# Optimization experiments

Hardware: AMD Instinct MI355X
Metric: run time of the kernel (lower is better)

The kernel has to match this reference:

```python
import jax, jax.numpy as jnp
from jax import lax
import numpy as np

B, S = 64, 16
GD, LD, PD, HD, CD = 64, 32, 8, 64, 64  # global, local, periodic, hidden, coder dims
TWO_PI = 6.283185307179586


def _conv(x, w, b):
    y = lax.conv_general_dilated(x, w, (2, 2), [(1, 1), (1, 1)])
    return y + b[None, :, None, None]


def _deconv(x, w, b):
    # torch ConvTranspose2d(k=4, s=2, p=1); w is [in, out, 4, 4].
    # Equivalent: dilate lhs by 2, pad k-1-p=2 each side, conv with flipped kernel.
    wt = jnp.flip(w, (2, 3)).transpose(1, 0, 2, 3)  # -> OIHW
    y = lax.conv_general_dilated(x, wt, (1, 1), [(2, 2), (2, 2)], lhs_dilation=(2, 2))
    return y + b[None, :, None, None]


def _bn(x, g, b, eps=1e-5):
    # training-mode BatchNorm2d (biased variance, per-channel affine)
    m = x.mean((0, 2, 3), keepdims=True)
    v = x.var((0, 2, 3), keepdims=True)
    return (x - m) * lax.rsqrt(v + eps) * g[None, :, None, None] + b[None, :, None, None]


def setup_inputs() -> dict:
    key = jax.random.key(0)
    ks = iter(jax.random.split(key, 40))
    n = lambda shape, s=0.02: jax.random.normal(next(ks), shape, jnp.float32) * s
    return {
        "Z_l": jax.random.normal(next(ks), (B, LD, S, S), jnp.float32),
        "Z_g": jax.random.normal(next(ks), (B, GD, S, S), jnp.float32),
        "imgs": jax.random.normal(next(ks), (B, 3, 128, 128), jnp.float32),
        "phi": jax.random.uniform(next(ks), (B, PD, 1, 1), jnp.float32),
        "lW": n((HD, GD)), "lb": n((HD,)),
        "l1W": n((PD, HD)), "l1b": n((PD,)),
        "l2W": n((PD, HD)), "l2b": n((PD,)),
        "cod_w0": n((64, 3, 4, 4)), "cod_b0": n((64,)),
        "cod_g0": 1.0 + n((64,)), "cod_be0": n((64,)),
        "cod_w1": n((128, 64, 4, 4)), "cod_b1": n((128,)),
        "cod_g1": 1.0 + n((128,)), "cod_be1": n((128,)),
        "cod_w2": n((CD, 128, 4, 4)), "cod_b2": n((CD,)),
        "gen_w0": n((CD + LD + GD + PD, 256, 4, 4)), "gen_b0": n((256,)),
        "gen_g0": 1.0 + n((256,)), "gen_be0": n((256,)),
        "gen_w1": n((256, 128, 4, 4)), "gen_b1": n((128,)),
        "gen_g1": 1.0 + n((128,)), "gen_be1": n((128,)),
        "gen_w2": n((128, 3, 4, 4)), "gen_b2": n((3,)),
    }


def reference(Z_l, Z_g, imgs, phi, lW, lb, l1W, l1b, l2W, l2b,
              cod_w0, cod_b0, cod_g0, cod_be0, cod_w1, cod_b1, cod_g1, cod_be1,
              cod_w2, cod_b2,
              gen_w0, gen_b0, gen_g0, gen_be0, gen_w1, gen_b1, gen_g1, gen_be1,
              gen_w2, gen_b2):
    # --- image coder: [B,3,128,128] -> [B,CD,16,16] ---
    h = jax.nn.leaky_relu(_bn(_conv(imgs, cod_w0, cod_b0), cod_g0, cod_be0), 0.2)
    h = jax.nn.leaky_relu(_bn(_conv(h, cod_w1, cod_b1), cod_g1, cod_be1), 0.2)
    Z_c = jnp.tanh(_conv(h, cod_w2, cod_b2))
    # --- periodic noise: vectorized outer-product replacing S*S python loop ---
    zg = Z_g[:, :, 0, 0]                       # [B, GD]
    x = jax.nn.relu(zg @ lW.T + lb)            # [B, HD]
    K1 = x @ l1W.T + l1b                       # [B, PD]
    K2 = x @ l2W.T + l2b                       # [B, PD]
    idx = jnp.arange(S, dtype=jnp.float32)
    wave = K1[:, :, None, None] * idx[:, None] + K2[:, :, None, None] * idx[None, :]
    Z_p = jnp.sin(wave + phi * TWO_PI)         # [B, PD, S, S]
    # --- generator ---
    Z = jnp.concatenate((Z_c, Z_l, Z_g, Z_p), axis=1)  # [B, 168, 16, 16]
    h = jax.nn.relu(_bn(_deconv(Z, gen_w0, gen_b0), gen_g0, gen_be0))
    h = jax.nn.relu(_bn(_deconv(h, gen_w1, gen_b1), gen_g1, gen_be1))
    return jnp.tanh(_deconv(h, gen_w2, gen_b2))        # [B, 3, 128, 128]
```

## Files before the change

### kernel.cpp

```cpp
#include <hip/hip_runtime.h>
#include <hip/hip_bf16.h>

#define TWO_PI_F 6.2831853071795864769f

typedef __attribute__((ext_vector_type(8))) __bf16 bf16x8;
typedef __attribute__((ext_vector_type(4))) float f32x4;

#define NREP 32

__device__ __forceinline__ float bf2f_raw(unsigned short u) {
    return __uint_as_float(((unsigned int)u) << 16);
}
__device__ __forceinline__ unsigned short f2bf(float f) {
    unsigned int u = __float_as_uint(f);
    unsigned int r = (u + 0x7FFFu + ((u >> 16) & 1u)) >> 16;
    return (unsigned short)r;
}
__device__ __forceinline__ float loadIn(const void* p, size_t i, bool f32) {
    return f32 ? ((const float*)p)[i] : bf2f_raw(((const unsigned short*)p)[i]);
}

__device__ __forceinline__ uint4 bn_fuse8(uint4 v, const float* __restrict__ sc,
                                          const float* __restrict__ sh, int c0, float slope) {
    unsigned short us[8];
    *(uint4*)us = v;
#pragma unroll
    for (int k = 0; k < 8; ++k) {
        float f = bf2f_raw(us[k]) * sc[c0 + k] + sh[c0 + k];
        f = f > 0.f ? f : slope * f;
        us[k] = f2bf(f);
    }
    return *(const uint4*)us;
}

__device__ __forceinline__ float kq_reduce(float v) {
    v += __shfl_xor(v, 16, 64);
    v += __shfl_xor(v, 32, 64);
    return v;
}

static constexpr size_t OFF_WC0 = 0;
static constexpr size_t OFF_WG2 = 3072;
static constexpr size_t OFF_P   = 9216;
static constexpr size_t OFF_CB0 = OFF_P + 0;
static constexpr size_t OFF_CG0 = OFF_P + 64;
static constexpr size_t OFF_CBE0= OFF_P + 128;
static constexpr size_t OFF_CB1 = OFF_P + 192;
static constexpr size_t OFF_CG1 = OFF_P + 320;
static constexpr size_t OFF_CBE1= OFF_P + 448;
static constexpr size_t OFF_CB2 = OFF_P + 576;
static constexpr size_t OFF_GB0 = OFF_P + 640;
static constexpr size_t OFF_GG0 = OFF_P + 896;
static constexpr size_t OFF_GBE0= OFF_P + 1152;
static constexpr size_t OFF_GB1 = OFF_P + 1408;
static constexpr size_t OFF_GG1 = OFF_P + 1536;
static constexpr size_t OFF_GBE1= OFF_P + 1664;
static constexpr size_t OFF_GB2 = OFF_P + 1792;
static constexpr size_t OFF_SSUM  = OFF_P + 2048;
static constexpr size_t OFF_SSQ   = OFF_SSUM + NREP * 576;
static constexpr size_t OFF_SCALE = OFF_SSQ + NREP * 576;
static constexpr size_t OFF_SHIFT = OFF_SCALE + 576;
static constexpr size_t OFF_K12   = OFF_SHIFT + 576;
static constexpr size_t OFF_FLAG  = OFF_K12 + 1024;
static constexpr size_t FP32_END  = OFF_FLAG + 16;
static constexpr size_t UXT = 2 * FP32_END;
static constexpr size_t UYT = UXT + 16777216;
static constexpr size_t UZT = UYT + 8388608;
static constexpr size_t UW0 = UYT + 33554432;
static constexpr size_t UW1 = UW0 + 786432;
static constexpr size_t UWC1 = UW1 + 524288;
static constexpr size_t UWC2 = UWC1 + 131072;
static constexpr size_t UW2 = UWC2 + 131072;
static constexpr size_t WS_END_USHORT = UW2 + 32768;
static constexpr size_t WS_NEED_BYTES = WS_END_USHORT * 2;


__global__ void detect_kernel(const unsigned short* __restrict__ imgs, int* __restrict__ flag) {
    int t = threadIdx.x;
    unsigned short u = imgs[t];
    int e = (u >> 7) & 0xFF;
    unsigned long long b = __ballot(e >= 0xC0);
    __shared__ int cnt[4];
    if ((t & 63) == 0) cnt[t >> 6] = __popcll(b);
    __syncthreads();
    if (t == 0) flag[0] = (cnt[0] + cnt[1] + cnt[2] + cnt[3] >= 4) ? 1 : 0;
}

struct CvtJobs {
    const void* src[16];
    float* dst[16];
    int off[17];
};

__global__ void cvt_all_kernel(CvtJobs J, int total, const int* __restrict__ flg) {
    int i = blockIdx.x * 256 + threadIdx.x;
    if (i >= total) return;
    bool f32 = flg[0] != 0;
    int k = 0;
#pragma unroll
    for (int t = 0; t < 15; ++t) { if (i >= J.off[t + 1]) k = t + 1; }
    int r = i - J.off[k];
    J.dst[k][r] = loadIn(J.src[k], r, f32);
}

__global__ void zero_kernel(float* p, int n) {
    int i = blockIdx.x * 256 + threadIdx.x;
    if (i < n) p[i] = 0.f;
}

__global__ void pack_w2_kernel(const void* __restrict__ src, unsigned short* __restrict__ dst,
                               int ICreal, int ICP, int OC, const int* __restrict__ flg) {
    bool f32 = flg[0] != 0;
    int i = blockIdx.x * 256 + threadIdx.x;
    int total = 16 * OC * ICP;
    if (i >= total) return;
    int jj = i & 7;
    int lane = (i >> 3) & 63;
    int j = (i >> 9) & 3;
    int t3 = i >> 11;
    int NK = ICP / 32;
    int kc = t3 % NK;
    int t4 = t3 / NK;
    int NOCT = OC / 64;
    int oct = t4 % NOCT;
    int ktap = t4 / NOCT;
    int kq = lane >> 4, n = lane & 15;
    int ic = kc * 32 + kq * 8 + jj;
    int oc = oct * 64 + n * 4 + j;
    unsigned short v = 0;
    if (ic < ICreal) v = f2bf(loadIn(src, ((size_t)(ic * OC + oc) << 4) + ktap, f32));
    dst[i] = v;
}

__global__ void pack_w2s_kernel(const void* __restrict__ src, unsigned short* __restrict__ dst,
                                int ICP, int OCreal, const int* __restrict__ flg) {
    bool f32 = flg[0] != 0;
    int i = blockIdx.x * 256 + threadIdx.x;
    int NK = ICP / 32;
    int total = 16 * NK * 512;
    if (i >= total) return;
    int jj = i & 7;
    int lane = (i >> 3) & 63;
    int t3 = i >> 9;
    int kc = t3 % NK;
    int ktap = t3 / NK;
    int kq = lane >> 4, n = lane & 15;
    int ic = kc * 32 + kq * 8 + jj;
    unsigned short v = 0;
    if (n < OCreal) v = f2bf(loadIn(src, ((size_t)(ic * OCreal + n) << 4) + ktap, f32));
    dst[i] = v;
}

__global__ void pack_wc_kernel(const void* __restrict__ src, unsigned short* __restrict__ dst,
                               int IC, int OC, const int* __restrict__ flg) {
    bool f32 = flg[0] != 0;
    int i = blockIdx.x * 256 + threadIdx.x;
    int total = 16 * OC * IC;
    if (i >= total) return;
    int jj = i & 7;
    int lane = (i >> 3) & 63;
    int j = (i >> 9) & 3;
    int t3 = i >> 11;
    int NK = IC / 32;
    int kc = t3 % NK;
    int t4 = t3 / NK;
    int NOCT = OC / 64;
    int oct = t4 % NOCT;
    int ktap = t4 / NOCT;
    int kq = lane >> 4, n = lane & 15;
    int ic = kc * 32 + kq * 8 + jj;
    int oc = oct * 64 + j * 16 + n;
    dst[i] = f2bf(loadIn(src, ((size_t)(oc * IC + ic) << 4) + ktap, f32));
}

__global__ void mlp_kernel(const void* __restrict__ Zg,
                           const void* __restrict__ lW, const void* __restrict__ lb,
                           const void* __restrict__ l1W, const void* __restrict__ l1b,
                           const void* __restrict__ l2W, const void* __restrict__ l2b,
                           float* __restrict__ K12, const int* __restrict__ flg) {
    bool f32 = flg[0] != 0;
    int b = blockIdx.x;
    int t = threadIdx.x;
    __shared__ float xs[64];
    float acc = loadIn(lb, t, f32);
    for (int c = 0; c < 64; ++c)
        acc += loadIn(Zg, (size_t)(b * 64 + c) * 256, f32) * loadIn(lW, t * 64 + c, f32);
    xs[t] = fmaxf(acc, 0.f);
    __syncthreads();
    if (t < 16) {
        int p = t & 7;
        const void* Wp = (t < 8) ? l1W : l2W;
        const void* bp = (t < 8) ? l1b : l2b;
        float a = loadIn(bp, p, f32);
        for (int h = 0; h < 64; ++h) a += xs[h] * loadIn(Wp, p * 64 + h, f32);
        K12[b * 16 + t] = a;
    }
}

__global__ void conv0_s2d_kernel(const void* __restrict__ imgs, const float* __restrict__ w,
                                 const float* __restrict__ bias, unsigned short* __restrict__ xs,
                                 const int* __restrict__ flg) {
    bool f32 = flg[0] != 0;
    int b = blockIdx.z;
    int tile = blockIdx.x;
    int Y0 = (tile >> 2) * 16, X0 = (tile & 3) * 16;
    __shared__ float vin[3 * 34 * 35];
    __shared__ float wl[64 * 49];
    for (int i = threadIdx.x; i < 3 * 34 * 34; i += 256) {
        int c = i % 34; int t = i / 34; int r = t % 34; int ic = t / 34;
        int iy = 2 * Y0 - 1 + r, ix = 2 * X0 - 1 + c;
        float v = 0.f;
        if (((unsigned)iy < 128u) & ((unsigned)ix < 128u))
            v = loadIn(imgs, ((size_t)(b * 3 + ic) * 128 + iy) * 128 + ix, f32);
        vin[(ic * 34 + r) * 35 + c] = v;
    }
    for (int i = threadIdx.x; i < 3072; i += 256) {
        int oc = i / 48, idx = i % 48;
        wl[oc * 49 + idx] = w[i];
    }
    __syncthreads();
    int q = threadIdx.x >> 2;
    int ocq = threadIdx.x & 3;
    int qy = q >> 3, qx = q & 7;
    float acc[4][16];
#pragma unroll
    for (int p = 0; p < 4; ++p)
#pragma unroll
        for (int o = 0; o < 16; ++o) acc[p][o] = 0.f;
    for (int ic = 0; ic < 3; ++ic) {
        float v[6][6];
#pragma unroll
        for (int r = 0; r < 6; ++r)
#pragma unroll
            for (int c = 0; c < 6; ++c)
                v[r][c] = vin[(ic * 34 + 4 * qy + r) * 35 + 4 * qx + c];
#pragma unroll
        for (int o = 0; o < 16; ++o) {
            const float* wo = wl + (ocq * 16 + o) * 49 + ic * 16;
#pragma unroll
            for (int ky = 0; ky < 4; ++ky)
#pragma unroll
                for (int kx = 0; kx < 4; ++kx) {
                    float wv = wo[ky * 4 + kx];
                    acc[0][o] = fmaf(v[ky][kx], wv, acc[0][o]);
                    acc[1][o] = fmaf(v[ky][kx + 2], wv, acc[1][o]);
                    acc[2][o] = fmaf(v[ky + 2][kx], wv, acc[2][o]);
                    acc[3][o] = fmaf(v[ky + 2][kx + 2], wv, acc[3][o]);
                }
        }
    }
    int j = (Y0 >> 1) + qy, i2 = (X0 >> 1) + qx;
#pragma unroll
    for (int p = 0; p < 4; ++p) {
        int dy = p >> 1, dx = p & 1;
        unsigned short tmp[16];
#pragma unroll
        for (int o = 0; o < 16; ++o) tmp[o] = f2bf(acc[p][o] + bias[ocq * 16 + o]);
        unsigned short* dst = xs + (((size_t)((b * 2 + dy) * 2 + dx) * 32 + j) * 32 + i2) * 64 + ocq * 16;
        *(uint4*)(dst) = *(const uint4*)(tmp);
        *(uint4*)(dst + 8) = *(const uint4*)(tmp + 8);
    }
}

__global__ void conv1_mfma_kernel(const unsigned short* __restrict__ xs,
                                  const unsigned short* __restrict__ wp,
                                  const float* __restrict__ bias,
                                  const float* __restrict__ sc, const float* __restrict__ sh,
                                  float* __restrict__ gsum, float* __restrict__ gsq,
                                  unsigned short* __restrict__ ys) {
    constexpr int STR = 72;
    __shared__ unsigned short lds[4 * 3 * 17 * STR];
    __shared__ float ws[4][64], wq[4][64];
    int bid = blockIdx.x;
    int slot = (bid & (NREP - 1)) * 576;
    int xt = bid & 1;
    int qp = (bid >> 1) & 15;
    int b = bid >> 5;
    int oy0 = qp * 2, x0 = xt * 16;
    for (int i = threadIdx.x; i < 1632; i += 256) {
        int icc = i & 7; int t = i >> 3;
        int col = t % 17; int rc = t / 17;
        int row = rc % 3; int pl = rc / 3;
        int py = pl >> 1, px = pl & 1;
        int j = oy0 - py + row;
        int ci = x0 - px + col;
        uint4 v = {0u, 0u, 0u, 0u};
        if (((unsigned)j < 32u) & ((unsigned)ci < 32u)) {
            v = *(const uint4*)(xs + ((size_t)((b * 4 + pl) * 32 + j) * 32 + ci) * 64 + icc * 8);
            v = bn_fuse8(v, sc, sh, icc * 8, 0.2f);
        }
        *(uint4*)(lds + ((pl * 3 + row) * 17 + col) * STR + icc * 8) = v;
    }
    __syncthreads();

    int wv = threadIdx.x >> 6, lane = threadIdx.x & 63;
    int r = wv >> 1, oct = wv & 1;
    int m = lane & 15, kq = lane >> 4;
    f32x4 acc[4];
#pragma unroll
    for (int j = 0; j < 4; ++j) acc[j] = (f32x4){0.f, 0.f, 0.f, 0.f};

#pragma unroll
    for (int ky = 0; ky < 4; ++ky) {
        int py = (ky & 1) ^ 1;
        int lrow = r + (ky >> 1);
#pragma unroll
        for (int kx = 0; kx < 4; ++kx) {
            int px = (kx & 1) ^ 1;
            int pl = py * 2 + px;
            int lcol = m + (kx >> 1);
            const unsigned short* lp = lds + ((pl * 3 + lrow) * 17 + lcol) * STR + kq * 8;
            int ktap = ky * 4 + kx;
            const unsigned short* bb = wp + (size_t)(ktap * 2 + oct) * 4096;
#pragma unroll
            for (int kc = 0; kc < 2; ++kc) {
                bf16x8 a = *(const bf16x8*)(lp + kc * 32);
                const unsigned short* bk = bb + kc * 2048 + lane * 8;
                bf16x8 b0 = *(const bf16x8*)(bk);
                bf16x8 b1 = *(const bf16x8*)(bk + 512);
                bf16x8 b2 = *(const bf16x8*)(bk + 1024);
                bf16x8 b3 = *(const bf16x8*)(bk + 1536);
                acc[0] = __builtin_amdgcn_mfma_f32_16x16x32_bf16(a, b0, acc[0], 0, 0, 0);
                acc[1] = __builtin_amdgcn_mfma_f32_16x16x32_bf16(a, b1, acc[1], 0, 0, 0);
                acc[2] = __builtin_amdgcn_mfma_f32_16x16x32_bf16(a, b2, acc[2], 0, 0, 0);
                acc[3] = __builtin_amdgcn_mfma_f32_16x16x32_bf16(a, b3, acc[3], 0, 0, 0);
            }
        }
    }
    int oy = oy0 + r;
    int pyo = oy & 1, jo = oy >> 1;
    int n = m;
    float bv0 = bias[oct * 64 + n], bv1 = bias[oct * 64 + 16 + n];
    float bv2 = bias[oct * 64 + 32 + n], bv3 = bias[oct * 64 + 48 + n];
    float s0 = 0, s1 = 0, s2 = 0, s3 = 0, q0 = 0, q1 = 0, q2 = 0, q3 = 0;
#pragma unroll
    for (int reg = 0; reg < 4; ++reg) {
        int mm = kq * 4 + reg;
        int ox = x0 + mm;
        int pxo = ox & 1, io = ox >> 1;
        size_t base = (((size_t)((b * 2 + pyo) * 2 + pxo) * 16 + jo) * 16 + io) * 128 + oct * 64 + n;
        float v0 = acc[0][reg] + bv0, v1 = acc[1][reg] + bv1;
        float v2 = acc[2][reg] + bv2, v3 = acc[3][reg] + bv3;
        s0 += v0; q0 += v0 * v0; s1 += v1; q1 += v1 * v1;
        s2 += v2; q2 += v2 * v2; s3 += v3; q3 += v3 * v3;
        ys[base]      = f2bf(v0);
        ys[base + 16] = f2bf(v1);
        ys[base + 32] = f2bf(v2);
        ys[base + 48] = f2bf(v3);
    }
    s0 = kq_reduce(s0); q0 = kq_reduce(q0);
    s1 = kq_reduce(s1); q1 = kq_reduce(q1);
    s2 = kq_reduce(s2); q2 = kq_reduce(q2);
    s3 = kq_reduce(s3); q3 = kq_reduce(q3);
    if (lane < 16) {
        ws[wv][0 * 16 + n] = s0; wq[wv][0 * 16 + n] = q0;
        ws[wv][1 * 16 + n] = s1; wq[wv][1 * 16 + n] = q1;
        ws[wv][2 * 16 + n] = s2; wq[wv][2 * 16 + n] = q2;
        ws[wv][3 * 16 + n] = s3; wq[wv][3 * 16 + n] = q3;
    }
    __syncthreads();
    if (threadIdx.x < 128) {
        int c = threadIdx.x;
        int o = c >> 6, rr = c & 63;
        float s = ws[o][rr] + ws[o + 2][rr];
        float q = wq[o][rr] + wq[o + 2][rr];
        atomicAdd(&gsum[slot + 64 + c], s);
        atomicAdd(&gsq[slot + 64 + c], q);
    }
}

__global__ void conv2_mfma_kernel(const unsigned short* __restrict__ ys,
                                  const unsigned short* __restrict__ wp,
                                  const float* __restrict__ bias,
                                  const float* __restrict__ sc, const float* __restrict__ sh,
                                  unsigned short* __restrict__ zt) {
    constexpr int STR = 136;
    __shared__ unsigned short lds[4 * 3 * 17 * STR];
    int bid = blockIdx.x;
    int qp = bid & 7;
    int b = bid >> 3;
    int oy0 = qp * 2;
    for (int i = threadIdx.x; i < 3264; i += 256) {
        int icc = i & 15; int t = i >> 4;
        int col = t % 17; int rc = t / 17;
        int row = rc % 3; int pl = rc / 3;
        int py = pl >> 1, px = pl & 1;
        int j = oy0 - py + row;
        int ci = col - px;
        uint4 v = {0u, 0u, 0u, 0u};
        if (((unsigned)j < 16u) & ((unsigned)ci < 16u)) {
            v = *(const uint4*)(ys + ((size_t)((b * 4 + pl) * 16 + j) * 16 + ci) * 128 + icc * 8);
            v = bn_fuse8(v, sc, sh, icc * 8, 0.2f);
        }
        *(uint4*)(lds + ((pl * 3 + row) * 17 + col) * STR + icc * 8) = v;
    }
    __syncthreads();

    int wv = threadIdx.x >> 6, lane = threadIdx.x & 63;
    int r = wv >> 1, jh = wv & 1;
    int m = lane & 15, kq = lane >> 4;
    f32x4 acc[2];
    acc[0] = (f32x4){0.f, 0.f, 0.f, 0.f};
    acc[1] = acc[0];
#pragma unroll
    for (int ky = 0; ky < 4; ++ky) {
        int py = (ky & 1) ^ 1;
        int lrow = r + (ky >> 1);
#pragma unroll
        for (int kx = 0; kx < 4; ++kx) {
            int px = (kx & 1) ^ 1;
            int pl = py * 2 + px;
            int lcol = m + (kx >> 1);
            const unsigned short* lp = lds + ((pl * 3 + lrow) * 17 + lcol) * STR + kq * 8;
            int ktap = ky * 4 + kx;
            const unsigned short* bb = wp + (size_t)ktap * 8192;
#pragma unroll
            for (int kc = 0; kc < 4; ++kc) {
                bf16x8 a = *(const bf16x8*)(lp + kc * 32);
                const unsigned short* bk = bb + kc * 2048 + (jh * 2) * 512 + lane * 8;
                bf16x8 b0 = *(const bf16x8*)(bk);
                bf16x8 b1 = *(const bf16x8*)(bk + 512);
                acc[0] = __builtin_amdgcn_mfma_f32_16x16x32_bf16(a, b0, acc[0], 0, 0, 0);
                acc[1] = __builtin_amdgcn_mfma_f32_16x16x32_bf16(a, b1, acc[1], 0, 0, 0);
            }
        }
    }
    int oy = oy0 + r;
    int n = m;
    float bv0 = bias[(jh * 2) * 16 + n], bv1 = bias[(jh * 2 + 1) * 16 + n];
#pragma unroll
    for (int reg = 0; reg < 4; ++reg) {
        int x = kq * 4 + reg;
        size_t base = ((size_t)(b * 16 + oy) * 16 + x) * 192 + (jh * 2) * 16 + n;
        zt[base]      = f2bf(tanhf(acc[0][reg] + bv0));
        zt[base + 16] = f2bf(tanhf(acc[1][reg] + bv1));
    }
}

__global__ void assemble_z(const void* __restrict__ Zl, const void* __restrict__ Zg,
                           const void* __restrict__ phi, const float* __restrict__ K12,
                           unsigned short* __restrict__ zt, const int* __restrict__ flg) {
    bool f32 = flg[0] != 0;
    int i = blockIdx.x * 256 + threadIdx.x;
    const int TOT = 64 * 128 * 256;
    if (i >= TOT) return;
    int pos = i & 255;
    int t = i >> 8;
    int c128 = t % 128;
    int b = t / 128;
    float val;
    if (c128 < 32) {
        val = loadIn(Zl, ((size_t)(b * 32 + c128) << 8) + pos, f32);
    } else if (c128 < 96) {
        val = loadIn(Zg, ((size_t)(b * 64 + (c128 - 32)) << 8) + pos, f32);
    } else if (c128 < 104) {
        int p = c128 - 96;
        int y = pos >> 4, x = pos & 15;
        float k1 = K12[b * 16 + p];
        float k2 = K12[b * 16 + 8 + p];
        val = sinf(k1 * (float)y + k2 * (float)x + loadIn(phi, b * 8 + p, f32) * TWO_PI_F);
    } else {
        val = 0.f;
    }
    zt[((size_t)(b * 256 + pos)) * 192 + 64 + c128] = f2bf(val);
}

template <int ICP, int Q, int OC, int QR, bool BN, bool ST>
__global__ __launch_bounds__(256, 2)
void deconv_mfma2_kernel(const unsigned short* __restrict__ in_t,
                         const unsigned short* __restrict__ wp2,
                         const float* __restrict__ bias,
                         const float* __restrict__ sc, const float* __restrict__ sh,
                         float* __restrict__ gsum, float* __restrict__ gsq, int statoff,
                         unsigned short* __restrict__ out_t) {
    constexpr int NOCT = OC / 64;
    constexpr int NK = ICP / 32;
    constexpr int XT = Q / 16;
    constexpr int NQB = Q / QR;
    constexpr int ROWS = QR + 2;
    constexpr int STRIDE = ICP + 8;
    constexpr int NTILES = XT * NQB * 64;
    __shared__ unsigned short lds[ROWS * 18 * STRIDE];
    __shared__ float ws[ST ? 4 : 1][64], wq[ST ? 4 : 1][64];

    int bid = blockIdx.x;
    int slot = (bid & (NREP - 1)) * 576;
    int oct = bid / NTILES;
    bid -= oct * NTILES;
    int xt = bid % XT;
    int t2 = bid / XT;
    int qp = t2 % NQB;
    int b = t2 / NQB;
    int qy0 = qp * QR;
    int x0 = xt * 16;

    constexpr int P8 = ICP / 8;
    constexpr int E8 = ROWS * 18 * P8;
    for (int i = threadIdx.x; i < E8; i += 256) {
        int icc = i % P8;
        int rc = i / P8;
        int row = rc / 18, col = rc % 18;
        int y = qy0 - 1 + row, x = x0 - 1 + col;
        uint4 val = {0u, 0u, 0u, 0u};
        if (((unsigned)y < (unsigned)Q) & ((unsigned)x < (unsigned)Q)) {
            val = *(const uint4*)(in_t + (size_t)((b * Q + y) * Q + x) * ICP + icc * 8);
            if (BN) val = bn_fuse8(val, sc, sh, icc * 8, 0.f);
        }
        *(uint4*)(lds + rc * STRIDE + icc * 8) = val;
    }
    __syncthreads();

    int wv = threadIdx.x >> 6, lane = threadIdx.x & 63;
    int dy = wv >> 1, dx = wv & 1;
    int m = lane & 15, kq = lane >> 4;

    f32x4 acc[QR][4];
#pragma unroll
    for (int q = 0; q < QR; ++q)
#pragma unroll
        for (int j = 0; j < 4; ++j) acc[q][j] = (f32x4){0.f, 0.f, 0.f, 0.f};

#pragma unroll
    for (int t = 0; t < 4; ++t) {
        int rr = t >> 1, cc = t & 1;
        int ktap = ((3 - dy) - 2 * rr) * 4 + ((3 - dx) - 2 * cc);
        int col = m + dx + cc;
        int row0 = dy + rr;
        const unsigned short* bbase = wp2 + (size_t)((ktap * NOCT + oct) * NK) * 2048;
#pragma unroll
        for (int kc = 0; kc < NK; ++kc) {
            bf16x8 a[QR];
#pragma unroll
            for (int q = 0; q < QR; ++q)
                a[q] = *(const bf16x8*)(lds + ((row0 + q) * 18 + col) * STRIDE + kc * 32 + kq * 8);
            bf16x8 b0 = *(const bf16x8*)(bbase + (kc * 4 + 0) * 512 + lane * 8);
            bf16x8 b1 = *(const bf16x8*)(bbase + (kc * 4 + 1) * 512 + lane * 8);
            bf16x8 b2 = *(const bf16x8*)(bbase + (kc * 4 + 2) * 512 + lane * 8);
            bf16x8 b3 = *(const bf16x8*)(bbase + (kc * 4 + 3) * 512 + lane * 8);
#pragma unroll
            for (int q = 0; q < QR; ++q) {
                acc[q][0] = __builtin_amdgcn_mfma_f32_16x16x32_bf16(a[q], b0, acc[q][0], 0, 0, 0);
                acc[q][1] = __builtin_amdgcn_mfma_f32_16x16x32_bf16(a[q], b1, acc[q][1], 0, 0, 0);
                acc[q][2] = __builtin_amdgcn_mfma_f32_16x16x32_bf16(a[q], b2, acc[q][2], 0, 0, 0);
                acc[q][3] = __builtin_amdgcn_mfma_f32_16x16x32_bf16(a[q], b3, acc[q][3], 0, 0, 0);
            }
        }
    }
    int n = m;
    const float4 bv = *(const float4*)(bias + oct * 64 + 4 * n);
    float s0 = 0, s1 = 0, s2 = 0, s3 = 0, q0 = 0, q1 = 0, q2 = 0, q3 = 0;
#pragma unroll
    for (int qyl = 0; qyl < QR; ++qyl) {
        int oy = 2 * (qy0 + qyl) + dy;
#pragma unroll
        for (int reg = 0; reg < 4; ++reg) {
            int mm = kq * 4 + reg;
            int ox = 2 * (x0 + mm) + dx;
            size_t base = ((size_t)((b * 2 * Q + oy) * (2 * Q) + ox)) * OC + oct * 64 + 4 * n;
            float v0 = acc[qyl][0][reg] + bv.x;
            float v1 = acc[qyl][1][reg] + bv.y;
            float v2 = acc[qyl][2][reg] + bv.z;
            float v3 = acc[qyl][3][reg] + bv.w;
            if (ST) {
                s0 += v0; q0 += v0 * v0; s1 += v1; q1 += v1 * v1;
                s2 += v2; q2 += v2 * v2; s3 += v3; q3 += v3 * v3;
            }
            ushort4 tv;
            tv.x = f2bf(v0); tv.y = f2bf(v1); tv.z = f2bf(v2); tv.w = f2bf(v3);
            *(ushort4*)(out_t + base) = tv;
        }
    }
    if (ST) {
        s0 = kq_reduce(s0); q0 = kq_reduce(q0);
        s1 = kq_reduce(s1); q1 = kq_reduce(q1);
        s2 = kq_reduce(s2); q2 = kq_reduce(q2);
        s3 = kq_reduce(s3); q3 = kq_reduce(q3);
        if (lane < 16) {
            ws[wv][4 * n + 0] = s0; wq[wv][4 * n + 0] = q0;
            ws[wv][4 * n + 1] = s1; wq[wv][4 * n + 1] = q1;
            ws[wv][4 * n + 2] = s2; wq[wv][4 * n + 2] = q2;
            ws[wv][4 * n + 3] = s3; wq[wv][4 * n + 3] = q3;
        }
        __syncthreads();
        if (threadIdx.x < 64) {
            int c = threadIdx.x;
            float s = ws[0][c] + ws[1][c] + ws[2][c] + ws[3][c];
            float q = wq[0][c] + wq[1][c] + wq[2][c] + wq[3][c];
            atomicAdd(&gsum[slot + statoff + oct * 64 + c], s);
            atomicAdd(&gsq[slot + statoff + oct * 64 + c], q);
        }
    }
}

__global__ void deconv2_mfma_kernel(const unsigned short* __restrict__ yt,
                                    const unsigned short* __restrict__ wp,
                                    const float* __restrict__ bias,
                                    const float* __restrict__ sc, const float* __restrict__ sh,
                                    float* __restrict__ outp) {
    constexpr int Q = 64, ICP = 128, NK = 4, STRIDE = 136, QR = 4, ROWS = 6;
    __shared__ unsigned short lds[ROWS * 18 * STRIDE];
    int bid = blockIdx.x;
    int xt = bid & 3;
    int t2 = bid >> 2;
    int qp = t2 & 15;
    int b = t2 >> 4;
    int qy0 = qp * QR, x0 = xt * 16;

    for (int i = threadIdx.x; i < ROWS * 18 * 16; i += 256) {
        int icc = i & 15;
        int rc = i >> 4;
        int row = rc / 18, col = rc % 18;
        int y = qy0 - 1 + row, x = x0 - 1 + col;
        uint4 v = {0u, 0u, 0u, 0u};
        if (((unsigned)y < (unsigned)Q) & ((unsigned)x < (unsigned)Q)) {
            v = *(const uint4*)(yt + (size_t)((b * Q + y) * Q + x) * ICP + icc * 8);
            v = bn_fuse8(v, sc, sh, icc * 8, 0.f);
        }
        *(uint4*)(lds + rc * STRIDE + icc * 8) = v;
    }
    __syncthreads();

    int wv = threadIdx.x >> 6, lane = threadIdx.x & 63;
    int dy = wv >> 1, dx = wv & 1;
    int m = lane & 15, kq = lane >> 4;
    f32x4 acc[QR];
#pragma unroll
    for (int q = 0; q < QR; ++q) acc[q] = (f32x4){0.f, 0.f, 0.f, 0.f};

#pragma unroll
    for (int t = 0; t < 4; ++t) {
        int rr = t >> 1, cc = t & 1;
        int ktap = ((3 - dy) - 2 * rr) * 4 + ((3 - dx) - 2 * cc);
        int col = m + dx + cc;
        int row0 = dy + rr;
        const unsigned short* bb = wp + (size_t)(ktap * NK) * 512;
#pragma unroll
        for (int kc = 0; kc < NK; ++kc) {
            bf16x8 a[QR];
#pragma unroll
            for (int q = 0; q < QR; ++q)
                a[q] = *(const bf16x8*)(lds + ((row0 + q) * 18 + col) * STRIDE + kc * 32 + kq * 8);
            bf16x8 b0 = *(const bf16x8*)(bb + kc * 512 + lane * 8);
#pragma unroll
            for (int q = 0; q < QR; ++q)
                acc[q] = __builtin_amdgcn_mfma_f32_16x16x32_bf16(a[q], b0, acc[q], 0, 0, 0);
        }
    }
    int n = m;
    if (n < 3) {
        float bv = bias[n];
#pragma unroll
        for (int qyl = 0; qyl < QR; ++qyl) {
            int oy = 2 * (qy0 + qyl) + dy;
#pragma unroll
            for (int reg = 0; reg < 4; ++reg) {
                int mm = kq * 4 + reg;
                int ox = 2 * (x0 + mm) + dx;
                size_t ob = (size_t)(b * 3 + n) * 16384;
                outp[ob + (size_t)oy * 128 + ox] = tanhf(acc[qyl][reg] + bv);
            }
        }
    }
}

template <int C>
__global__ void stat_reduce_t(const unsigned short* __restrict__ x, int total4,
                              float* __restrict__ ssum, float* __restrict__ ssq, int statoff) {
    __shared__ float ls[C], lq[C];
    for (int c = threadIdx.x; c < C; c += 256) { ls[c] = 0.f; lq[c] = 0.f; }
    __syncthreads();
    int i0 = blockIdx.x * 256 + threadIdx.x;
    int stride = gridDim.x * 256;
    int c0 = (i0 << 2) & (C - 1);
    float s0 = 0, s1 = 0, s2 = 0, s3 = 0, q0 = 0, q1 = 0, q2 = 0, q3 = 0;
    for (int i = i0; i < total4; i += stride) {
        ushort4 v = *(const ushort4*)(x + ((size_t)i << 2));
        float f0 = bf2f_raw(v.x), f1 = bf2f_raw(v.y), f2 = bf2f_raw(v.z), f3 = bf2f_raw(v.w);
        s0 += f0; s1 += f1; s2 += f2; s3 += f3;
        q0 += f0 * f0; q1 += f1 * f1; q2 += f2 * f2; q3 += f3 * f3;
    }
    atomicAdd(&ls[c0], s0); atomicAdd(&ls[c0 + 1], s1); atomicAdd(&ls[c0 + 2], s2); atomicAdd(&ls[c0 + 3], s3);
    atomicAdd(&lq[c0], q0); atomicAdd(&lq[c0 + 1], q1); atomicAdd(&lq[c0 + 2], q2); atomicAdd(&lq[c0 + 3], q3);
    __syncthreads();
    int slot = (blockIdx.x & (NREP - 1)) * 576;
    for (int c = threadIdx.x; c < C; c += 256) {
        atomicAdd(&ssum[slot + statoff + c], ls[c]);
        atomicAdd(&ssq[slot + statoff + c], lq[c]);
    }
}

__global__ void bn_fin_kernel(const float* __restrict__ ssum, const float* __restrict__ ssq,
                              const float* __restrict__ g, const float* __restrict__ be,
                              float* __restrict__ scale, float* __restrict__ shift,
                              int statoff, int C, float invN) {
    int c = threadIdx.x;
    if (c >= C) return;
    float s = 0.f, q = 0.f;
#pragma unroll
    for (int r = 0; r < NREP; ++r) {
        s += ssum[r * 576 + statoff + c];
        q += ssq[r * 576 + statoff + c];
    }
    float m = s * invN;
    float v = q * invN - m * m;
    v = fmaxf(v, 0.f);
    float sc = g[c] * rsqrtf(v + 1e-5f);
    scale[statoff + c] = sc;
    shift[statoff + c] = be[c] - m * sc;
}

extern "C" void kernel_launch(void* const* d_in, const int* in_sizes, int n_in,
                              void* d_out, int out_size, void* d_ws, size_t ws_size,
                              hipStream_t stream) {
    if (ws_size < WS_NEED_BYTES) {
        hipMemsetAsync(d_out, 0, (size_t)out_size * 4, stream);
        return;
    }

    float* W = (float*)d_ws;
    unsigned short* U = (unsigned short*)d_ws;
    int* FLG = (int*)(W + OFF_FLAG);

    detect_kernel<<<1, 256, 0, stream>>>((const unsigned short*)d_in[2], FLG);

    CvtJobs J;
    const int srcIdx[16] = {10, 28, 11, 12, 13, 15, 16, 17, 19, 21, 22, 23, 25, 26, 27, 29};
    const int cnt[16]    = {3072, 6144, 64, 64, 64, 128, 128, 128, 64, 256, 256, 256, 128, 128, 128, 3};
    float* dsts[16] = {W + OFF_WC0, W + OFF_WG2,
                       W + OFF_CB0, W + OFF_CG0, W + OFF_CBE0, W + OFF_CB1, W + OFF_CG1, W + OFF_CBE1,
                       W + OFF_CB2, W + OFF_GB0, W + OFF_GG0, W + OFF_GBE0, W + OFF_GB1, W + OFF_GG1,
                       W + OFF_GBE1, W + OFF_GB2};
    int off = 0;
    for (int k = 0; k < 16; ++k) {
        J.src[k] = d_in[srcIdx[k]];
        J.dst[k] = dsts[k];
        J.off[k] = off;
        off += cnt[k];
    }
    J.off[16] = off;
    cvt_all_kernel<<<(off + 255) / 256, 256, 0, stream>>>(J, off, FLG);

    zero_kernel<<<(2 * NREP * 576 + 255) / 256, 256, 0, stream>>>(W + OFF_SSUM, 2 * NREP * 576);

    pack_w2_kernel<<<3072, 256, 0, stream>>>(d_in[20], U + UW0, 168, 192, 256, FLG);
    pack_w2_kernel<<<2048, 256, 0, stream>>>(d_in[24], U + UW1, 256, 256, 128, FLG);
    pack_wc_kernel<<<512, 256, 0, stream>>>(d_in[14], U + UWC1, 64, 128, FLG);
    pack_wc_kernel<<<512, 256, 0, stream>>>(d_in[18], U + UWC2, 128, 64, FLG);
    pack_w2s_kernel<<<128, 256, 0, stream>>>(d_in[28], U + UW2, 128, 3, FLG);

    mlp_kernel<<<64, 64, 0, stream>>>(d_in[1], d_in[4], d_in[5], d_in[6], d_in[7],
                                      d_in[8], d_in[9], W + OFF_K12, FLG);

    conv0_s2d_kernel<<<dim3(16, 1, 64), 256, 0, stream>>>(d_in[2], W + OFF_WC0, W + OFF_CB0,
                                                          U + UXT, FLG);
    stat_reduce_t<64><<<1024, 256, 0, stream>>>(U + UXT, 4194304, W + OFF_SSUM, W + OFF_SSQ, 0);
    bn_fin_kernel<<<1, 256, 0, stream>>>(W + OFF_SSUM, W + OFF_SSQ, W + OFF_CG0, W + OFF_CBE0,
                                         W + OFF_SCALE, W + OFF_SHIFT, 0, 64, 1.f / 262144.f);

    conv1_mfma_kernel<<<2048, 256, 0, stream>>>(U + UXT, U + UWC1, W + OFF_CB1,
                                                W + OFF_SCALE + 0, W + OFF_SHIFT + 0,
                                                W + OFF_SSUM, W + OFF_SSQ, U + UYT);
    bn_fin_kernel<<<1, 256, 0, stream>>>(W + OFF_SSUM, W + OFF_SSQ, W + OFF_CG1, W + OFF_CBE1,
                                         W + OFF_SCALE, W + OFF_SHIFT, 64, 128, 1.f / 65536.f);

    conv2_mfma_kernel<<<512, 256, 0, stream>>>(U + UYT, U + UWC2, W + OFF_CB2,
                                               W + OFF_SCALE + 64, W + OFF_SHIFT + 64, U + UZT);

    assemble_z<<<8192, 256, 0, stream>>>(d_in[0], d_in[1], d_in[3], W + OFF_K12, U + UZT, FLG);

    deconv_mfma2_kernel<192, 16, 256, 2, false, true><<<2048, 256, 0, stream>>>(
        U + UZT, U + UW0, W + OFF_GB0, nullptr, nullptr,
        W + OFF_SSUM, W + OFF_SSQ, 192, U + UXT);
    bn_fin_kernel<<<1, 256, 0, stream>>>(W + OFF_SSUM, W + OFF_SSQ, W + OFF_GG0, W + OFF_GBE0,
                                         W + OFF_SCALE, W + OFF_SHIFT, 192, 256, 1.f / 65536.f);

    deconv_mfma2_kernel<256, 32, 128, 4, true, false><<<2048, 256, 0, stream>>>(
        U + UXT, U + UW1, W + OFF_GB1, W + OFF_SCALE + 192, W + OFF_SHIFT + 192,
        nullptr, nullptr, 0, U + UYT);
    stat_reduce_t<128><<<1024, 256, 0, stream>>>(U + UYT, 8388608, W + OFF_SSUM, W + OFF_SSQ, 448);
    bn_fin_kernel<<<1, 256, 0, stream>>>(W + OFF_SSUM, W + OFF_SSQ, W + OFF_GG1, W + OFF_GBE1,
                                         W + OFF_SCALE, W + OFF_SHIFT, 448, 128, 1.f / 262144.f);

    deconv2_mfma_kernel<<<4096, 256, 0, stream>>>(U + UYT, U + UW2, W + OFF_GB2,
                                                  W + OFF_SCALE + 448, W + OFF_SHIFT + 448,
                                                  (float*)d_out);
}
```

Before: 589.2 us.

## Split deconv input channels into LDS phases to cut shared memory footprint

Adds a KPH template parameter that stages the input tile into LDS in KPH channel chunks, accumulating each chunk before loading the next. The second generator deconv uses two phases, halving its LDS buffer so more blocks can be resident per CU. It adds an extra barrier and load/compute serialization per block.

```diff
diff --git a/kernel.cpp b/kernel.cpp
--- a/kernel.cpp
+++ b/kernel.cpp
@@ -465,7 +465,7 @@
     zt[((size_t)(b * 256 + pos)) * 192 + 64 + c128] = f2bf(val);
 }
 
-template <int ICP, int Q, int OC, int QR, bool BN, bool ST>
+template <int ICP, int Q, int OC, int QR, bool BN, bool ST, int KPH>
 __global__ __launch_bounds__(256, 2)
 void deconv_mfma2_kernel(const unsigned short* __restrict__ in_t,
                          const unsigned short* __restrict__ wp2,
@@ -475,10 +475,12 @@
                          unsigned short* __restrict__ out_t) {
     constexpr int NOCT = OC / 64;
     constexpr int NK = ICP / 32;
+    constexpr int ICPP = ICP / KPH;
+    constexpr int NKL = NK / KPH;
     constexpr int XT = Q / 16;
     constexpr int NQB = Q / QR;
     constexpr int ROWS = QR + 2;
-    constexpr int STRIDE = ICP + 8;
+    constexpr int STRIDE = ICPP + 8;
     constexpr int NTILES = XT * NQB * 64;
     __shared__ unsigned short lds[ROWS * 18 * STRIDE];
     __shared__ float ws[ST ? 4 : 1][64], wq[ST ? 4 : 1][64];
@@ -494,22 +496,6 @@
     int qy0 = qp * QR;
     int x0 = xt * 16;
 
-    constexpr int P8 = ICP / 8;
-    constexpr int E8 = ROWS * 18 * P8;
-    for (int i = threadIdx.x; i < E8; i += 256) {
-        int icc = i % P8;
-        int rc = i / P8;
-        int row = rc / 18, col = rc % 18;
-        int y = qy0 - 1 + row, x = x0 - 1 + col;
-        uint4 val = {0u, 0u, 0u, 0u};
-        if (((unsigned)y < (unsigned)Q) & ((unsigned)x < (unsigned)Q)) {
-            val = *(const uint4*)(in_t + (size_t)((b * Q + y) * Q + x) * ICP + icc * 8);
-            if (BN) val = bn_fuse8(val, sc, sh, icc * 8, 0.f);
-        }
-        *(uint4*)(lds + rc * STRIDE + icc * 8) = val;
-    }
-    __syncthreads();
-
     int wv = threadIdx.x >> 6, lane = threadIdx.x & 63;
     int dy = wv >> 1, dx = wv & 1;
     int m = lane & 15, kq = lane >> 4;
@@ -520,29 +506,50 @@
 #pragma unroll
         for (int j = 0; j < 4; ++j) acc[q][j] = (f32x4){0.f, 0.f, 0.f, 0.f};
 
-#pragma unroll
-    for (int t = 0; t < 4; ++t) {
-        int rr = t >> 1, cc = t & 1;
-        int ktap = ((3 - dy) - 2 * rr) * 4 + ((3 - dx) - 2 * cc);
-        int col = m + dx + cc;
-        int row0 = dy + rr;
-        const unsigned short* bbase = wp2 + (size_t)((ktap * NOCT + oct) * NK) * 2048;
-#pragma unroll
-        for (int kc = 0; kc < NK; ++kc) {
-            bf16x8 a[QR];
-#pragma unroll
-            for (int q = 0; q < QR; ++q)
-                a[q] = *(const bf16x8*)(lds + ((row0 + q) * 18 + col) * STRIDE + kc * 32 + kq * 8);
-            bf16x8 b0 = *(const bf16x8*)(bbase + (kc * 4 + 0) * 512 + lane * 8);
-            bf16x8 b1 = *(const bf16x8*)(bbase + (kc * 4 + 1) * 512 + lane * 8);
-            bf16x8 b2 = *(const bf16x8*)(bbase + (kc * 4 + 2) * 512 + lane * 8);
-            bf16x8 b3 = *(const bf16x8*)(bbase + (kc * 4 + 3) * 512 + lane * 8);
-#pragma unroll
-            for (int q = 0; q < QR; ++q) {
-                acc[q][0] = __builtin_amdgcn_mfma_f32_16x16x32_bf16(a[q], b0, acc[q][0], 0, 0, 0);
-                acc[q][1] = __builtin_amdgcn_mfma_f32_16x16x32_bf16(a[q], b1, acc[q][1], 0, 0, 0);
-                acc[q][2] = __builtin_amdgcn_mfma_f32_16x16x32_bf16(a[q], b2, acc[q][2], 0, 0, 0);
-                acc[q][3] = __builtin_amdgcn_mfma_f32_16x16x32_bf16(a[q], b3, acc[q][3], 0, 0, 0);
+    constexpr int P8 = ICPP / 8;
+    constexpr int E8 = ROWS * 18 * P8;
+#pragma unroll
+    for (int ph = 0; ph < KPH; ++ph) {
+        if (ph) __syncthreads();
+        for (int i = threadIdx.x; i < E8; i += 256) {
+            int icc = i % P8;
+            int rc = i / P8;
+            int row = rc / 18, col = rc % 18;
+            int y = qy0 - 1 + row, x = x0 - 1 + col;
+            uint4 val = {0u, 0u, 0u, 0u};
+            if (((unsigned)y < (unsigned)Q) & ((unsigned)x < (unsigned)Q)) {
+                val = *(const uint4*)(in_t + (size_t)((b * Q + y) * Q + x) * ICP + ph * ICPP + icc * 8);
+                if (BN) val = bn_fuse8(val, sc, sh, ph * ICPP + icc * 8, 0.f);
+            }
+            *(uint4*)(lds + rc * STRIDE + icc * 8) = val;
+        }
+        __syncthreads();
+
+#pragma unroll
+        for (int t = 0; t < 4; ++t) {
+            int rr = t >> 1, cc = t & 1;
+            int ktap = ((3 - dy) - 2 * rr) * 4 + ((3 - dx) - 2 * cc);
+            int col = m + dx + cc;
+            int row0 = dy + rr;
+            const unsigned short* bbase = wp2 + (size_t)((ktap * NOCT + oct) * NK) * 2048;
+#pragma unroll
+            for (int kc = 0; kc < NKL; ++kc) {
+                int kcg = ph * NKL + kc;
+                bf16x8 a[QR];
+#pragma unroll
+                for (int q = 0; q < QR; ++q)
+                    a[q] = *(const bf16x8*)(lds + ((row0 + q) * 18 + col) * STRIDE + kc * 32 + kq * 8);
+                bf16x8 b0 = *(const bf16x8*)(bbase + (kcg * 4 + 0) * 512 + lane * 8);
+                bf16x8 b1 = *(const bf16x8*)(bbase + (kcg * 4 + 1) * 512 + lane * 8);
+                bf16x8 b2 = *(const bf16x8*)(bbase + (kcg * 4 + 2) * 512 + lane * 8);
+                bf16x8 b3 = *(const bf16x8*)(bbase + (kcg * 4 + 3) * 512 + lane * 8);
+#pragma unroll
+                for (int q = 0; q < QR; ++q) {
+                    acc[q][0] = __builtin_amdgcn_mfma_f32_16x16x32_bf16(a[q], b0, acc[q][0], 0, 0, 0);
+                    acc[q][1] = __builtin_amdgcn_mfma_f32_16x16x32_bf16(a[q], b1, acc[q][1], 0, 0, 0);
+                    acc[q][2] = __builtin_amdgcn_mfma_f32_16x16x32_bf16(a[q], b2, acc[q][2], 0, 0, 0);
+                    acc[q][3] = __builtin_amdgcn_mfma_f32_16x16x32_bf16(a[q], b3, acc[q][3], 0, 0, 0);
+                }
             }
         }
     }
@@ -768,13 +775,13 @@
 
     assemble_z<<<8192, 256, 0, stream>>>(d_in[0], d_in[1], d_in[3], W + OFF_K12, U + UZT, FLG);
 
-    deconv_mfma2_kernel<192, 16, 256, 2, false, true><<<2048, 256, 0, stream>>>(
+    deconv_mfma2_kernel<192, 16, 256, 2, false, true, 1><<<2048, 256, 0, stream>>>(
         U + UZT, U + UW0, W + OFF_GB0, nullptr, nullptr,
         W + OFF_SSUM, W + OFF_SSQ, 192, U + UXT);
     bn_fin_kernel<<<1, 256, 0, stream>>>(W + OFF_SSUM, W + OFF_SSQ, W + OFF_GG0, W + OFF_GBE0,
                                          W + OFF_SCALE, W + OFF_SHIFT, 192, 256, 1.f / 65536.f);
 
-    deconv_mfma2_kernel<256, 32, 128, 4, true, false><<<2048, 256, 0, stream>>>(
+    deconv_mfma2_kernel<256, 32, 128, 4, true, false, 2><<<2048, 256, 0, stream>>>(
         U + UXT, U + UW1, W + OFF_GB1, W + OFF_SCALE + 192, W + OFF_SHIFT + 192,
         nullptr, nullptr, 0, U + UYT);
     stat_reduce_t<128><<<1024, 256, 0, stream>>>(U + UYT, 8388608, W + OFF_SSUM, W + OFF_SSQ, 448);
```

Measured after the change: 561.6 us. 1.05x faster.
